# Optimization experiments

Hardware: AMD Instinct MI355X
Metric: run time of the kernel (lower is better)

The kernel has to match this reference:

```python
import jax, jax.numpy as jnp
import numpy as np

_HIST_BINS = 64
TOP_K_FRAC = 0.125
HIST_THRESHOLD = 2048


def setup_inputs() -> dict:
    key = jax.random.key(0)
    B, S = 256, 131072
    importance = jax.random.normal(key, (B, S), dtype=jnp.float32)
    return {"importance": importance, "S": S}


def reference(importance, S):
    # importance: [B, S] float32; S: python int
    K = max(1, int(TOP_K_FRAC * S))
    if S > HIST_THRESHOLD:
        # Histogram bookkeeping path (computed but unused by the original module;
        # reproduced here for faithfulness to the source's memory traffic).
        imin = jnp.min(importance, axis=-1, keepdims=True)  # [B,1]
        imax = jnp.max(importance, axis=-1, keepdims=True)  # [B,1]
        rng = jnp.clip(imax - imin, 1e-8, None)
        bin_idx = ((importance - imin) / rng * (_HIST_BINS - 1)).astype(jnp.int32)
        bin_idx = jnp.clip(bin_idx, 0, _HIST_BINS - 1)  # [B,S]
        B = importance.shape[0]
        rows = jnp.arange(B)[:, None]  # [B,1] broadcast against [B,S]
        hist = jnp.zeros((B, _HIST_BINS), dtype=jnp.int32).at[rows, bin_idx].add(1)
        del hist  # dead value, exactly as in the torch source
    _, top_idx = jax.lax.top_k(importance, K)  # [B,K] indices into last dim
    return (top_idx, K)
```

## Files before the change

kernel.cpp:

```cpp
#include <hip/hip_runtime.h>
#include <stdint.h>


#define S_LEN   131072
#define K_SEL   16384
#define NBINS   8192
#define LOWBITS 19
#define IDXMASK 0x1FFFFu
#define NCH_H   4
#define HCHUNK  (S_LEN / NCH_H)
#define NCH_G   8
#define GCHUNK  (S_LEN / NCH_G)
#define CAND_CAP 20480
#define SORT_CAP 4096
#define DIRECT_MAX 256
#define WL_PER_ROW 2048
#define D_GRID  2048

__device__ __forceinline__ unsigned int ordered_u32(float f) {
  unsigned int x = __float_as_uint(f);
  unsigned int mask = (unsigned int)((int)x >> 31) | 0x80000000u;
  return x ^ mask;
}

__global__ __launch_bounds__(1024)
void hist_kernel(const float* __restrict__ in, unsigned int* __restrict__ histA) {
  const int row = blockIdx.x / NCH_H;
  const int ch  = blockIdx.x % NCH_H;
  const int tid = threadIdx.x;
  __shared__ unsigned int h[NBINS];
  for (int i = tid; i < NBINS; i += 1024) h[i] = 0;
  __syncthreads();
  const float4* p = (const float4*)(in + (size_t)row * S_LEN + (size_t)ch * HCHUNK);
#pragma unroll 8
  for (int it = 0; it < HCHUNK / 4 / 1024; ++it) {
    float4 v = p[it * 1024 + tid];
    atomicAdd(&h[ordered_u32(v.x) >> LOWBITS], 1u);
    atomicAdd(&h[ordered_u32(v.y) >> LOWBITS], 1u);
    atomicAdd(&h[ordered_u32(v.z) >> LOWBITS], 1u);
    atomicAdd(&h[ordered_u32(v.w) >> LOWBITS], 1u);
  }
  __syncthreads();
  unsigned int* dst = histA + (size_t)blockIdx.x * NBINS;
  for (int i = tid; i < NBINS; i += 1024) dst[i] = h[i];
}

__global__ __launch_bounds__(1024)
void scan_kernel(const unsigned int* __restrict__ histA, unsigned int* __restrict__ arr,
                 unsigned int* __restrict__ meta, uint4* __restrict__ wl,
                 unsigned int* __restrict__ ctrs, unsigned int wlHalf,
                 int* __restrict__ out, int B, long long out_size) {
  const int row  = blockIdx.x;
  const int tid  = threadIdx.x;
  const int lane = tid & 63, wave = tid >> 6;
  __shared__ unsigned int sfx[NBINS];
  __shared__ unsigned int waveTot[16];
  __shared__ unsigned int sb1;
  const unsigned int* h0 = histA + (size_t)(row * NCH_H) * NBINS;

  unsigned int v[8];
#pragma unroll
  for (int s = 0; s < 8; ++s) {
    int b = tid * 8 + s;
    v[s] = h0[b] + h0[NBINS + b] + h0[2 * NBINS + b] + h0[3 * NBINS + b];
  }
#pragma unroll
  for (int s = 6; s >= 0; --s) v[s] += v[s + 1];
  unsigned int tot = v[0];
  unsigned int suf = tot;
#pragma unroll
  for (int d = 1; d < 64; d <<= 1) {
    unsigned int o = __shfl_down(suf, d, 64);
    if (lane + d < 64) suf += o;
  }
  if (lane == 0) waveTot[wave] = suf;
  __syncthreads();
  unsigned int carry = 0;
  for (int w2 = wave + 1; w2 < 16; ++w2) carry += waveTot[w2];
  unsigned int addv = (suf - tot) + carry;
#pragma unroll
  for (int s = 0; s < 8; ++s) sfx[tid * 8 + s] = v[s] + addv;
  __syncthreads();
#pragma unroll
  for (int s = 0; s < 8; ++s) {
    int b = tid * 8 + s;
    unsigned int cur = sfx[b];
    unsigned int nxt = (b + 1 < NBINS) ? sfx[b + 1] : 0u;
    if (cur >= K_SEL && nxt < K_SEL) sb1 = (unsigned int)b;
  }
  __syncthreads();
  const unsigned int b1 = sb1;
  unsigned int* a = arr + (size_t)row * NBINS;
  for (int i = tid; i < NBINS; i += 1024) a[i] = sfx[i];
  for (unsigned int b = b1 + (unsigned int)tid; b < NBINS; b += 1024) {
    unsigned int end   = sfx[b];
    unsigned int start = (b + 1 < NBINS) ? sfx[b + 1] : 0u;
    unsigned int cnt   = end - start;
    if (cnt) {
      if (cnt > DIRECT_MAX) {
        unsigned int pos = atomicAdd(&ctrs[0], 1u);
        if (pos < wlHalf) wl[2 * wlHalf - 1 - pos] = make_uint4((unsigned int)row, start, end, 0u);
      } else {
        unsigned int pos = atomicAdd(&ctrs[1], 1u);
        if (pos < wlHalf) wl[pos] = make_uint4((unsigned int)row, start, end, 0u);
      }
    }
  }
  if (tid == 0) {
    meta[row] = b1;
    if (row == 0) {
      long long pos = (long long)B * K_SEL;
      if (pos < out_size) out[pos] = K_SEL;
    }
  }
}

__global__ __launch_bounds__(1024)
void gather_kernel(const float* __restrict__ in, unsigned int* __restrict__ arr,
                   const unsigned int* __restrict__ meta,
                   unsigned long long* __restrict__ cand) {
  const int row   = blockIdx.x / NCH_G;
  const int chunk = blockIdx.x % NCH_G;
  const int tid   = threadIdx.x;
  const unsigned int b1 = meta[row];
  unsigned int* a = arr + (size_t)row * NBINS;
  unsigned long long* c = cand + (size_t)row * CAND_CAP;
  const int base = chunk * GCHUNK;
  const float4* p = (const float4*)(in + (size_t)row * S_LEN + base);

  __shared__ unsigned int hcnt[NBINS];
  for (int i = tid; i < NBINS; i += 1024) hcnt[i] = 0;
  __syncthreads();
#pragma unroll 4
  for (int it = 0; it < GCHUNK / 4 / 1024; ++it) {
    float4 v = p[it * 1024 + tid];
    float f[4] = {v.x, v.y, v.z, v.w};
#pragma unroll
    for (int e = 0; e < 4; ++e) {
      unsigned int b = ordered_u32(f[e]) >> LOWBITS;
      if (b >= b1) atomicAdd(&hcnt[b], 1u);
    }
  }
  __syncthreads();
  for (unsigned int b = b1 + (unsigned int)tid; b < NBINS; b += 1024) {
    unsigned int cnt = hcnt[b];
    if (cnt) hcnt[b] = atomicSub(&a[b], cnt) - cnt;
  }
  __syncthreads();
#pragma unroll 4
  for (int it = 0; it < GCHUNK / 4 / 1024; ++it) {
    int i4 = it * 1024 + tid;
    float4 v = p[i4];
    int idx0 = base + i4 * 4;
    float f[4] = {v.x, v.y, v.z, v.w};
#pragma unroll
    for (int e = 0; e < 4; ++e) {
      unsigned int u = ordered_u32(f[e]);
      unsigned int b = u >> LOWBITS;
      if (b >= b1) {
        unsigned int pos = atomicAdd(&hcnt[b], 1u);
        unsigned long long key =
            ((unsigned long long)u << 17) |
            (unsigned long long)(IDXMASK - (unsigned int)(idx0 + e));
        if (pos < CAND_CAP) c[pos] = key;
      }
    }
  }
}

__global__ __launch_bounds__(256)
void sort_kernel(const uint4* __restrict__ wl, const unsigned int* __restrict__ ctrs,
                 unsigned int wlHalf, const unsigned long long* __restrict__ cand,
                 int* __restrict__ out) {
  const int tid  = threadIdx.x;
  const int lane = tid & 63, wave = tid >> 6;
  __shared__ unsigned int   skey2[SORT_CAP];
  __shared__ unsigned char  sdig2[SORT_CAP];
  __shared__ unsigned int   ssfx[257];
  __shared__ unsigned int   scur[256];
  __shared__ unsigned int   segTot[4];
  unsigned int nHeavy = ctrs[0]; if (nHeavy > wlHalf) nHeavy = wlHalf;
  unsigned int nLight = ctrs[1]; if (nLight > wlHalf) nLight = wlHalf;

  for (unsigned int w = blockIdx.x; w < nHeavy; w += gridDim.x) {
    const uint4 it = wl[2 * wlHalf - 1 - w];
    const unsigned int row = it.x, start = it.y;
    unsigned int count = it.z - start;
    if (count > SORT_CAP) count = SORT_CAP;
    const unsigned long long* c = cand + (size_t)row * CAND_CAP + start;
    int* orow = out + (size_t)row * K_SEL;

    scur[tid] = 0;
    __syncthreads();
    for (unsigned int i = tid; i < count; i += 256)
      atomicAdd(&scur[(unsigned int)(c[i] >> 28) & 255u], 1u);
    __syncthreads();
    unsigned int cnt = scur[tid];
    unsigned int suf = cnt;
#pragma unroll
    for (int d = 1; d < 64; d <<= 1) {
      unsigned int o = __shfl_down(suf, d, 64);
      if (lane + d < 64) suf += o;
    }
    if (lane == 0) segTot[wave] = suf;
    __syncthreads();
    unsigned int carry = 0;
    for (int w2 = wave + 1; w2 < 4; ++w2) carry += segTot[w2];
    ssfx[tid] = suf + carry;
    if (tid == 0) ssfx[256] = 0;
    __syncthreads();
    scur[tid] = ssfx[tid + 1];
    __syncthreads();
    for (unsigned int i = tid; i < count; i += 256) {
      unsigned long long k = c[i];
      unsigned int d = (unsigned int)(k >> 28) & 255u;
      unsigned int p = atomicAdd(&scur[d], 1u);
      skey2[p] = (unsigned int)k & 0x0FFFFFFFu;
      sdig2[p] = (unsigned char)d;
    }
    __syncthreads();
    for (unsigned int p = tid; p < count; p += 256) {
      unsigned int k = skey2[p];
      unsigned int d = sdig2[p];
      unsigned int lo = ssfx[d + 1], hi = ssfx[d];
      unsigned int r = 0;
      for (unsigned int q = lo; q < hi; ++q) r += (skey2[q] > k) ? 1u : 0u;
      unsigned int pos = start + lo + r;
      if (pos < K_SEL)
        orow[pos] = (int)(IDXMASK - (k & IDXMASK));
    }
    __syncthreads();
  }

  for (unsigned int w = blockIdx.x * 4u + (unsigned int)wave; w < nLight;
       w += gridDim.x * 4u) {
    const uint4 it = wl[w];
    const unsigned int row = it.x, start = it.y;
    const unsigned int count = it.z - start;
    const unsigned long long* c = cand + (size_t)row * CAND_CAP + start;
    int* orow = out + (size_t)row * K_SEL;
    unsigned long long me[4];
#pragma unroll
    for (int e = 0; e < 4; ++e) {
      unsigned int i = (unsigned int)lane + 64u * e;
      me[e] = (i < count) ? c[i] : 0ull;
    }
    unsigned int r[4] = {0u, 0u, 0u, 0u};
#pragma unroll
    for (int e = 0; e < 4; ++e) {
      for (int l = 0; l < 64; ++l) {
        unsigned long long kj = __shfl(me[e], l, 64);
#pragma unroll
        for (int e2 = 0; e2 < 4; ++e2) r[e2] += (kj > me[e2]) ? 1u : 0u;
      }
    }
#pragma unroll
    for (int e = 0; e < 4; ++e) {
      unsigned int i = (unsigned int)lane + 64u * e;
      if (i < count) {
        unsigned int pos = start + r[e];
        if (pos < K_SEL)
          orow[pos] = (int)(IDXMASK - ((unsigned int)me[e] & IDXMASK));
      }
    }
  }
}

extern "C" void kernel_launch(void* const* d_in, const int* in_sizes, int n_in,
                              void* d_out, int out_size, void* d_ws, size_t ws_size,
                              hipStream_t stream) {
  const float* importance = (const float*)d_in[0];
  int B = in_sizes[0] / S_LEN;
  if (B < 1) B = 1;
  (void)n_in; (void)ws_size;

  const unsigned int wlCap  = (unsigned int)B * WL_PER_ROW;
  const unsigned int wlHalf = wlCap / 2;
  size_t histBytes = (size_t)B * NCH_H * NBINS * sizeof(unsigned int);
  size_t arrBytes  = (size_t)B * NBINS * sizeof(unsigned int);
  size_t candBytes = (size_t)B * CAND_CAP * sizeof(unsigned long long);
  size_t wlBytes   = (size_t)wlCap * sizeof(uint4);
  char* base = (char*)d_ws;
  unsigned int* histA      = (unsigned int*)base;
  unsigned int* arr        = (unsigned int*)(base + histBytes);
  unsigned long long* cand = (unsigned long long*)(base + histBytes + arrBytes);
  uint4* wl                = (uint4*)(base + histBytes + arrBytes + candBytes);
  unsigned int* meta       = (unsigned int*)(base + histBytes + arrBytes + candBytes + wlBytes);
  unsigned int* ctrs       = meta + B;
  int* out = (int*)d_out;

  hipMemsetAsync(ctrs, 0, 4 * sizeof(unsigned int), stream);
  hist_kernel  <<<dim3(B * NCH_H), dim3(1024), 0, stream>>>(importance, histA);
  scan_kernel  <<<dim3(B),         dim3(1024), 0, stream>>>(
      histA, arr, meta, wl, ctrs, wlHalf, out, B, (long long)out_size);
  gather_kernel<<<dim3(B * NCH_G), dim3(1024), 0, stream>>>(importance, arr, meta, cand);
  sort_kernel  <<<dim3(D_GRID),    dim3(256),  0, stream>>>(wl, ctrs, wlHalf, cand, out);
}
```

Baseline: 300.8 us.

## Fuse histogram, scan and gather into one per-row select kernel

Replaces the separate hist, scan and gather kernels with a single kernel that uses one block per row. That block builds the full-row histogram in shared memory, scans it, buffers worklist entries locally before reserving global slots in bulk, and scatters candidates with shared-memory offsets. This removes the global histogram and offset arrays, the per-chunk counting pass, and two kernel launches. The cost is parallelism: only B=256 blocks each stream a whole 512KB row, with heavy LDS use, so occupancy and bandwidth may suffer on a 256-CU device.

```diff
diff --git a/kernel.cpp b/kernel.cpp
--- a/kernel.cpp
+++ b/kernel.cpp
@@ -7,15 +7,14 @@
 #define NBINS   8192
 #define LOWBITS 19
 #define IDXMASK 0x1FFFFu
-#define NCH_H   4
-#define HCHUNK  (S_LEN / NCH_H)
-#define NCH_G   8
-#define GCHUNK  (S_LEN / NCH_G)
 #define CAND_CAP 20480
 #define SORT_CAP 4096
 #define DIRECT_MAX 256
 #define WL_PER_ROW 2048
 #define D_GRID  2048
+#define HCAP 256
+#define LCAP 2048
+#define NITER (S_LEN / 4 / 1024)
 
 __device__ __forceinline__ unsigned int ordered_u32(float f) {
   unsigned int x = __float_as_uint(f);
@@ -24,46 +23,39 @@
 }
 
 __global__ __launch_bounds__(1024)
-void hist_kernel(const float* __restrict__ in, unsigned int* __restrict__ histA) {
-  const int row = blockIdx.x / NCH_H;
-  const int ch  = blockIdx.x % NCH_H;
-  const int tid = threadIdx.x;
-  __shared__ unsigned int h[NBINS];
-  for (int i = tid; i < NBINS; i += 1024) h[i] = 0;
-  __syncthreads();
-  const float4* p = (const float4*)(in + (size_t)row * S_LEN + (size_t)ch * HCHUNK);
-#pragma unroll 8
-  for (int it = 0; it < HCHUNK / 4 / 1024; ++it) {
-    float4 v = p[it * 1024 + tid];
-    atomicAdd(&h[ordered_u32(v.x) >> LOWBITS], 1u);
-    atomicAdd(&h[ordered_u32(v.y) >> LOWBITS], 1u);
-    atomicAdd(&h[ordered_u32(v.z) >> LOWBITS], 1u);
-    atomicAdd(&h[ordered_u32(v.w) >> LOWBITS], 1u);
-  }
-  __syncthreads();
-  unsigned int* dst = histA + (size_t)blockIdx.x * NBINS;
-  for (int i = tid; i < NBINS; i += 1024) dst[i] = h[i];
-}
-
-__global__ __launch_bounds__(1024)
-void scan_kernel(const unsigned int* __restrict__ histA, unsigned int* __restrict__ arr,
-                 unsigned int* __restrict__ meta, uint4* __restrict__ wl,
-                 unsigned int* __restrict__ ctrs, unsigned int wlHalf,
-                 int* __restrict__ out, int B, long long out_size) {
+void select_kernel(const float* __restrict__ in,
+                   unsigned long long* __restrict__ cand,
+                   uint4* __restrict__ wl, unsigned int* __restrict__ ctrs,
+                   unsigned int wlHalf, int* __restrict__ out,
+                   int B, long long out_size) {
   const int row  = blockIdx.x;
   const int tid  = threadIdx.x;
   const int lane = tid & 63, wave = tid >> 6;
+  __shared__ unsigned int h[NBINS];
   __shared__ unsigned int sfx[NBINS];
   __shared__ unsigned int waveTot[16];
-  __shared__ unsigned int sb1;
-  const unsigned int* h0 = histA + (size_t)(row * NCH_H) * NBINS;
-
-  unsigned int v[8];
-#pragma unroll
-  for (int s = 0; s < 8; ++s) {
-    int b = tid * 8 + s;
-    v[s] = h0[b] + h0[NBINS + b] + h0[2 * NBINS + b] + h0[3 * NBINS + b];
-  }
+  __shared__ unsigned int sb1, nH, nL, gHs, gLs;
+  __shared__ uint2 lheavy[HCAP];
+  __shared__ uint2 llight[LCAP];
+
+  for (int i = tid; i < NBINS; i += 1024) h[i] = 0;
+  if (tid == 0) { nH = 0; nL = 0; }
+  __syncthreads();
+
+  const float4* p = (const float4*)(in + (size_t)row * S_LEN);
+#pragma unroll 8
+  for (int it = 0; it < NITER; ++it) {
+    float4 v4 = p[it * 1024 + tid];
+    atomicAdd(&h[ordered_u32(v4.x) >> LOWBITS], 1u);
+    atomicAdd(&h[ordered_u32(v4.y) >> LOWBITS], 1u);
+    atomicAdd(&h[ordered_u32(v4.z) >> LOWBITS], 1u);
+    atomicAdd(&h[ordered_u32(v4.w) >> LOWBITS], 1u);
+  }
+  __syncthreads();
+
+  uint4 c0 = *(const uint4*)&h[tid * 8];
+  uint4 c1 = *(const uint4*)&h[tid * 8 + 4];
+  unsigned int v[8] = {c0.x, c0.y, c0.z, c0.w, c1.x, c1.y, c1.z, c1.w};
 #pragma unroll
   for (int s = 6; s >= 0; --s) v[s] += v[s + 1];
   unsigned int tot = v[0];
@@ -78,8 +70,12 @@
   unsigned int carry = 0;
   for (int w2 = wave + 1; w2 < 16; ++w2) carry += waveTot[w2];
   unsigned int addv = (suf - tot) + carry;
-#pragma unroll
-  for (int s = 0; s < 8; ++s) sfx[tid * 8 + s] = v[s] + addv;
+  {
+    uint4 o0 = make_uint4(v[0] + addv, v[1] + addv, v[2] + addv, v[3] + addv);
+    uint4 o1 = make_uint4(v[4] + addv, v[5] + addv, v[6] + addv, v[7] + addv);
+    *(uint4*)&sfx[tid * 8]     = o0;
+    *(uint4*)&sfx[tid * 8 + 4] = o1;
+  }
   __syncthreads();
 #pragma unroll
   for (int s = 0; s < 8; ++s) {
@@ -90,81 +86,74 @@
   }
   __syncthreads();
   const unsigned int b1 = sb1;
-  unsigned int* a = arr + (size_t)row * NBINS;
-  for (int i = tid; i < NBINS; i += 1024) a[i] = sfx[i];
-  for (unsigned int b = b1 + (unsigned int)tid; b < NBINS; b += 1024) {
-    unsigned int end   = sfx[b];
-    unsigned int start = (b + 1 < NBINS) ? sfx[b + 1] : 0u;
-    unsigned int cnt   = end - start;
-    if (cnt) {
-      if (cnt > DIRECT_MAX) {
-        unsigned int pos = atomicAdd(&ctrs[0], 1u);
-        if (pos < wlHalf) wl[2 * wlHalf - 1 - pos] = make_uint4((unsigned int)row, start, end, 0u);
-      } else {
-        unsigned int pos = atomicAdd(&ctrs[1], 1u);
-        if (pos < wlHalf) wl[pos] = make_uint4((unsigned int)row, start, end, 0u);
-      }
-    }
-  }
+
+  for (int i = tid; i < NBINS; i += 1024) {
+    unsigned int end   = sfx[i];
+    unsigned int start = (i + 1 < NBINS) ? sfx[i + 1] : 0u;
+    h[i] = start;
+    if ((unsigned int)i >= b1) {
+      unsigned int cnt = end - start;
+      if (cnt) {
+        if (cnt > DIRECT_MAX) {
+          unsigned int p2 = atomicAdd(&nH, 1u);
+          if (p2 < HCAP) lheavy[p2] = make_uint2(start, end);
+          else {
+            unsigned int g = atomicAdd(&ctrs[0], 1u);
+            if (g < wlHalf) wl[2 * wlHalf - 1 - g] = make_uint4((unsigned int)row, start, end, 0u);
+          }
+        } else {
+          unsigned int p2 = atomicAdd(&nL, 1u);
+          if (p2 < LCAP) llight[p2] = make_uint2(start, end);
+          else {
+            unsigned int g = atomicAdd(&ctrs[1], 1u);
+            if (g < wlHalf) wl[g] = make_uint4((unsigned int)row, start, end, 0u);
+          }
+        }
+      }
+    }
+  }
+  __syncthreads();
   if (tid == 0) {
-    meta[row] = b1;
-    if (row == 0) {
-      long long pos = (long long)B * K_SEL;
-      if (pos < out_size) out[pos] = K_SEL;
-    }
-  }
-}
-
-__global__ __launch_bounds__(1024)
-void gather_kernel(const float* __restrict__ in, unsigned int* __restrict__ arr,
-                   const unsigned int* __restrict__ meta,
-                   unsigned long long* __restrict__ cand) {
-  const int row   = blockIdx.x / NCH_G;
-  const int chunk = blockIdx.x % NCH_G;
-  const int tid   = threadIdx.x;
-  const unsigned int b1 = meta[row];
-  unsigned int* a = arr + (size_t)row * NBINS;
+    gHs = atomicAdd(&ctrs[0], nH < HCAP ? nH : HCAP);
+    gLs = atomicAdd(&ctrs[1], nL < LCAP ? nL : LCAP);
+  }
+  __syncthreads();
+  {
+    unsigned int hN = nH < HCAP ? nH : HCAP;
+    unsigned int lN = nL < LCAP ? nL : LCAP;
+    for (unsigned int i = tid; i < hN; i += 1024) {
+      uint2 e = lheavy[i]; unsigned int pos = gHs + i;
+      if (pos < wlHalf) wl[2 * wlHalf - 1 - pos] = make_uint4((unsigned int)row, e.x, e.y, 0u);
+    }
+    for (unsigned int i = tid; i < lN; i += 1024) {
+      uint2 e = llight[i]; unsigned int pos = gLs + i;
+      if (pos < wlHalf) wl[pos] = make_uint4((unsigned int)row, e.x, e.y, 0u);
+    }
+  }
+
   unsigned long long* c = cand + (size_t)row * CAND_CAP;
-  const int base = chunk * GCHUNK;
-  const float4* p = (const float4*)(in + (size_t)row * S_LEN + base);
-
-  __shared__ unsigned int hcnt[NBINS];
-  for (int i = tid; i < NBINS; i += 1024) hcnt[i] = 0;
-  __syncthreads();
 #pragma unroll 4
-  for (int it = 0; it < GCHUNK / 4 / 1024; ++it) {
-    float4 v = p[it * 1024 + tid];
-    float f[4] = {v.x, v.y, v.z, v.w};
-#pragma unroll
-    for (int e = 0; e < 4; ++e) {
-      unsigned int b = ordered_u32(f[e]) >> LOWBITS;
-      if (b >= b1) atomicAdd(&hcnt[b], 1u);
-    }
-  }
-  __syncthreads();
-  for (unsigned int b = b1 + (unsigned int)tid; b < NBINS; b += 1024) {
-    unsigned int cnt = hcnt[b];
-    if (cnt) hcnt[b] = atomicSub(&a[b], cnt) - cnt;
-  }
-  __syncthreads();
-#pragma unroll 4
-  for (int it = 0; it < GCHUNK / 4 / 1024; ++it) {
+  for (int it = 0; it < NITER; ++it) {
     int i4 = it * 1024 + tid;
-    float4 v = p[i4];
-    int idx0 = base + i4 * 4;
-    float f[4] = {v.x, v.y, v.z, v.w};
+    float4 v4 = p[i4];
+    int idx0 = i4 * 4;
+    float f[4] = {v4.x, v4.y, v4.z, v4.w};
 #pragma unroll
     for (int e = 0; e < 4; ++e) {
       unsigned int u = ordered_u32(f[e]);
       unsigned int b = u >> LOWBITS;
       if (b >= b1) {
-        unsigned int pos = atomicAdd(&hcnt[b], 1u);
+        unsigned int pos = atomicAdd(&h[b], 1u);
         unsigned long long key =
             ((unsigned long long)u << 17) |
             (unsigned long long)(IDXMASK - (unsigned int)(idx0 + e));
         if (pos < CAND_CAP) c[pos] = key;
       }
     }
+  }
+  if (row == 0 && tid == 0) {
+    long long pos = (long long)B * K_SEL;
+    if (pos < out_size) out[pos] = K_SEL;
   }
 }
 
@@ -276,23 +265,16 @@
 
   const unsigned int wlCap  = (unsigned int)B * WL_PER_ROW;
   const unsigned int wlHalf = wlCap / 2;
-  size_t histBytes = (size_t)B * NCH_H * NBINS * sizeof(unsigned int);
-  size_t arrBytes  = (size_t)B * NBINS * sizeof(unsigned int);
   size_t candBytes = (size_t)B * CAND_CAP * sizeof(unsigned long long);
   size_t wlBytes   = (size_t)wlCap * sizeof(uint4);
   char* base = (char*)d_ws;
-  unsigned int* histA      = (unsigned int*)base;
-  unsigned int* arr        = (unsigned int*)(base + histBytes);
-  unsigned long long* cand = (unsigned long long*)(base + histBytes + arrBytes);
-  uint4* wl                = (uint4*)(base + histBytes + arrBytes + candBytes);
-  unsigned int* meta       = (unsigned int*)(base + histBytes + arrBytes + candBytes + wlBytes);
-  unsigned int* ctrs       = meta + B;
+  unsigned long long* cand = (unsigned long long*)base;
+  uint4* wl                = (uint4*)(base + candBytes);
+  unsigned int* ctrs       = (unsigned int*)(base + candBytes + wlBytes);
   int* out = (int*)d_out;
 
   hipMemsetAsync(ctrs, 0, 4 * sizeof(unsigned int), stream);
-  hist_kernel  <<<dim3(B * NCH_H), dim3(1024), 0, stream>>>(importance, histA);
-  scan_kernel  <<<dim3(B),         dim3(1024), 0, stream>>>(
-      histA, arr, meta, wl, ctrs, wlHalf, out, B, (long long)out_size);
-  gather_kernel<<<dim3(B * NCH_G), dim3(1024), 0, stream>>>(importance, arr, meta, cand);
-  sort_kernel  <<<dim3(D_GRID),    dim3(256),  0, stream>>>(wl, ctrs, wlHalf, cand, out);
-}
+  select_kernel<<<dim3(B),      dim3(1024), 0, stream>>>(
+      importance, cand, wl, ctrs, wlHalf, out, B, (long long)out_size);
+  sort_kernel  <<<dim3(D_GRID), dim3(256),  0, stream>>>(wl, ctrs, wlHalf, cand, out);
+}
```

After: 272.6 us. 9.4% less time.
